# Optimization experiments

Hardware: AMD Instinct MI355X
Metric: run time of the kernel (lower is better)

## Reference

```python
import jax, jax.numpy as jnp
import numpy as np

N = 50000      # nodes
E = 800000     # edges
T = 3          # npass
ED = 64        # embedding_dim
NS = 23        # nshifts (arange(0.8, 3.0+1e-5, 0.1))
MD = NS + ED   # message_dim = 87
H = 200        # hidden width (hardcoded in module)
NMOL = 2048    # number of molecules (segments for final scatter)
RD = ED * (T + 1)  # readout input dim = 256
EPS = 1e-5

SHIFTS = jnp.asarray(np.arange(0.8, 3.0 + 1e-5, 0.1, dtype=np.float32))  # [23]


def setup_inputs() -> dict:
    key = jax.random.key(0)
    ks = jax.random.split(key, 32)
    inp = {
        'z_i': jax.random.randint(ks[0], (N,), 0, 10),
        'edge_index': jax.random.randint(ks[1], (2, E), 0, N),
        'dist_ij': jax.random.uniform(ks[2], (E, 1), dtype=jnp.float32) * 2.2 + 0.8,
        'mol_ind': jnp.sort(jax.random.randint(ks[3], (N,), 0, NMOL)),
        'emb': jax.random.normal(ks[4], (10, ED), dtype=jnp.float32),
        # per-pass update MLP params, stacked over T
        'up_bn_g': jnp.ones((T, MD), jnp.float32),
        'up_bn_b': jnp.zeros((T, MD), jnp.float32),
        'up_w1': jax.random.normal(ks[5], (T, MD, H), jnp.float32) * 0.05,
        'up_b1': jnp.zeros((T, H), jnp.float32),
        'up_w2': jax.random.normal(ks[6], (T, H, H), jnp.float32) * 0.05,
        'up_b2': jnp.zeros((T, H), jnp.float32),
        'up_w3': jax.random.normal(ks[7], (T, H, H), jnp.float32) * 0.05,
        'up_b3': jnp.zeros((T, H), jnp.float32),
        'up_w4': jax.random.normal(ks[8], (T, H, ED), jnp.float32) * 0.05,
        'up_b4': jnp.zeros((T, ED), jnp.float32),
        # readout MLP params
        'ro_bn_g': jnp.ones((RD,), jnp.float32),
        'ro_bn_b': jnp.zeros((RD,), jnp.float32),
        'ro_w1': jax.random.normal(ks[9], (RD, H), jnp.float32) * 0.05,
        'ro_b1': jnp.zeros((H,), jnp.float32),
        'ro_w2': jax.random.normal(ks[10], (H, H), jnp.float32) * 0.05,
        'ro_b2': jnp.zeros((H,), jnp.float32),
        'ro_w3': jax.random.normal(ks[11], (H, H), jnp.float32) * 0.05,
        'ro_b3': jnp.zeros((H,), jnp.float32),
        'ro_w4': jax.random.normal(ks[12], (H, 1), jnp.float32) * 0.05,
        'ro_b4': jnp.zeros((1,), jnp.float32),  # bias filled to 0 in __init__
    }
    return inp


def batchnorm(x, g, b):
    # BatchNorm1d in training mode: batch statistics, biased variance
    mu = jnp.mean(x, axis=0)
    var = jnp.mean(jnp.square(x - mu), axis=0)
    return (x - mu) * jax.lax.rsqrt(var + EPS) * g + b


def mlp(x, g, b, w1, b1, w2, b2, w3, b3, w4, b4):
    x = batchnorm(x, g, b)
    x = jax.nn.relu(x @ w1 + b1)
    x = jax.nn.relu(x @ w2 + b2)
    x = jax.nn.relu(x @ w3 + b3)
    return x @ w4 + b4


def reference(z_i, edge_index, dist_ij, mol_ind, emb,
              up_bn_g, up_bn_b, up_w1, up_b1, up_w2, up_b2, up_w3, up_b3, up_w4, up_b4,
              ro_bn_g, ro_bn_b, ro_w1, ro_b1, ro_w2, ro_b2, ro_w3, ro_b3, ro_w4, ro_b4):
    e_source, e_sink = edge_index[0], edge_index[1]
    rbf_ij = jnp.exp(-jnp.square(dist_ij - SHIFTS[None, :]))  # [E, NS]
    x_i = emb[z_i]                                            # [N, ED]
    x_list = [x_i]
    for t in range(T):
        m_ij = jnp.concatenate([rbf_ij, x_i[e_sink]], axis=1)  # [E, MD] gather
        m_i = jax.ops.segment_sum(m_ij, e_source, num_segments=N)  # scatter-sum
        x_i = x_i + 0.1 * mlp(m_i, up_bn_g[t], up_bn_b[t],
                              up_w1[t], up_b1[t], up_w2[t], up_b2[t],
                              up_w3[t], up_b3[t], up_w4[t], up_b4[t])
        x_list.append(x_i)
    x_all = jnp.concatenate(x_list, axis=1)  # [N, RD]
    y_i = mlp(x_all, ro_bn_g, ro_bn_b, ro_w1, ro_b1, ro_w2, ro_b2, ro_w3, ro_b3, ro_w4, ro_b4)
    y = jax.ops.segment_sum(y_i, mol_ind, num_segments=NMOL)  # [NMOL, 1]
    return y
```

## Files before the change

### kernel.cpp

```cpp
#include <hip/hip_runtime.h>
#include <hip/hip_bf16.h>
#include <type_traits>

#define NN 50000
#define NP 50048
#define EE 800000
#define TT 3
#define ED 64
#define NS 23
#define MD 87
#define HH 200
#define NMOL 2048
#define RD 256

#define SW 232
#define NPB2 512
#define SNB ((NN + 255) / 256)

typedef __attribute__((ext_vector_type(8))) short short8b;
typedef __attribute__((ext_vector_type(4))) float f32x4;

template <int V> using ic = std::integral_constant<int, V>;

__device__ __forceinline__ unsigned short f2bf(float f) {
  unsigned u = __float_as_uint(f);
  return (unsigned short)((u + 0x7fffu + ((u >> 16) & 1u)) >> 16);
}
__device__ __forceinline__ float ubf2f(unsigned short h) {
  return __uint_as_float(((unsigned)h) << 16);
}
__device__ __forceinline__ float bfp2f(unsigned p) {
  return __uint_as_float(p << 16) + __uint_as_float(p & 0xffff0000u);
}
__device__ __forceinline__ unsigned packsplit(float v) {
  unsigned short h = f2bf(v);
  unsigned short l = f2bf(v - ubf2f(h));
  return (unsigned)h | ((unsigned)l << 16);
}

struct WD { const float* src; short* dst; int K, N, Kpad, Npad, T; };
struct WDs { WD d[5]; };

__global__ __launch_bounds__(256) void wprep_kernel(WDs W) {
  WD w = W.d[blockIdx.y];
  int KB = w.Kpad >> 5, NT = w.Npad >> 4;
  int per = w.Npad * w.Kpad;
  int total = w.T * per;
  for (int idx = blockIdx.x * 256 + threadIdx.x; idx < total; idx += gridDim.x * 256) {
    int t = idx / per;
    int r = idx - t * per;
    int e = r & 7, lane = (r >> 3) & 63;
    int blk = r >> 9;
    int kb = blk % KB, tile = blk / KB;
    int ln = lane & 15, quad = lane >> 4;
    int n = tile * 16 + ln, k = kb * 32 + quad * 8 + e;
    float v = 0.f;
    if (k < w.K && n < w.N) v = w.src[((size_t)t * w.K + k) * w.N + n];
    unsigned short h = f2bf(v);
    unsigned short l = f2bf(v - ubf2f(h));
    size_t base = ((size_t)(t * NT + tile) * KB + kb) * 1024;
    w.dst[base + lane * 8 + e] = (short)h;
    w.dst[base + 512 + lane * 8 + e] = (short)l;
  }
}

__global__ __launch_bounds__(256) void wscale_kernel(const float* __restrict__ wsrc,
                                                     const float* __restrict__ na,
                                                     const float* __restrict__ nb,
                                                     const float* __restrict__ bsrc,
                                                     int K, int Kpad,
                                                     short* __restrict__ wsp,
                                                     float* __restrict__ bc) {
  int n = blockIdx.x;
  int k = threadIdx.x;
  int KB = Kpad >> 5;
  int tile = n >> 4, ln = n & 15;
  float contrib = 0.f;
  if (k < Kpad) {
    float v = 0.f;
    if (n < HH && k < K) {
      float w = wsrc[(size_t)k * HH + n];
      v = na[k] * w;
      contrib = nb[k] * w;
    }
    unsigned short h = f2bf(v);
    unsigned short l = f2bf(v - ubf2f(h));
    int kb = k >> 5, quad = (k & 31) >> 3, e = k & 7;
    int lane = quad * 16 + ln;
    size_t base = ((size_t)tile * KB + kb) * 1024;
    wsp[base + lane * 8 + e] = (short)h;
    wsp[base + 512 + lane * 8 + e] = (short)l;
  }
  __shared__ float sh[256];
  sh[k] = contrib;
  __syncthreads();
  for (int off = 128; off > 0; off >>= 1) {
    if (k < off) sh[k] += sh[k + off];
    __syncthreads();
  }
  if (k == 0) bc[n] = (n < HH ? bsrc[n] : 0.f) + sh[0];
}

__global__ __launch_bounds__(256) void emb_kernel(const int* __restrict__ z,
                                                  const float* __restrict__ emb,
                                                  unsigned* __restrict__ xp,
                                                  short* __restrict__ xq,
                                                  short* __restrict__ xqs) {
  int idx = blockIdx.x * 256 + threadIdx.x;
  if (idx >= NN * ED) return;
  int i = idx >> 6, d = idx & 63;
  unsigned pk = packsplit(emb[z[i] * ED + d]);
  xp[(size_t)i * RD + d] = pk;
  short h = (short)(pk & 0xffffu);
  xq[(size_t)i * RD + d] = h;
  xqs[(size_t)i * ED + d] = h;
}

__global__ __launch_bounds__(256) void hist_kernel(const int* __restrict__ src,
                                                   int* __restrict__ deg) {
  int e = blockIdx.x * 256 + threadIdx.x;
  if (e < EE) atomicAdd(&deg[src[e]], 1);
}

__global__ __launch_bounds__(256) void scanA_kernel(const int* __restrict__ deg,
                                                    int* __restrict__ Psum) {
  int i = blockIdx.x * 256 + threadIdx.x;
  int v = (i < NN) ? deg[i] : 0;
#pragma unroll
  for (int off = 32; off > 0; off >>= 1) v += __shfl_down(v, off, 64);
  __shared__ int ws[4];
  if ((threadIdx.x & 63) == 0) ws[threadIdx.x >> 6] = v;
  __syncthreads();
  if (threadIdx.x == 0) Psum[blockIdx.x] = ws[0] + ws[1] + ws[2] + ws[3];
}

__global__ __launch_bounds__(256) void scanB_kernel(const int* __restrict__ Psum,
                                                    int* __restrict__ Poff) {
  __shared__ int sh[256];
  int t = threadIdx.x;
  int v = (t < SNB) ? Psum[t] : 0;
  sh[t] = v;
  __syncthreads();
  for (int off = 1; off < 256; off <<= 1) {
    int u = (t >= off) ? sh[t - off] : 0;
    __syncthreads();
    sh[t] += u;
    __syncthreads();
  }
  if (t < SNB) Poff[t] = sh[t] - v;
}

__global__ __launch_bounds__(256) void scanC_kernel(const int* __restrict__ deg,
                                                    const int* __restrict__ Poff,
                                                    int* __restrict__ offs,
                                                    int* __restrict__ cursor) {
  __shared__ int sh[256];
  int t = threadIdx.x;
  int i = blockIdx.x * 256 + t;
  int v = (i < NN) ? deg[i] : 0;
  sh[t] = v;
  __syncthreads();
  for (int off = 1; off < 256; off <<= 1) {
    int u = (t >= off) ? sh[t - off] : 0;
    __syncthreads();
    sh[t] += u;
    __syncthreads();
  }
  int excl = Poff[blockIdx.x] + sh[t] - v;
  if (i < NN) {
    offs[i] = excl;
    cursor[i] = excl;
    if (i == NN - 1) offs[NN] = excl + v;
  }
}

__global__ __launch_bounds__(256) void scatter_kernel(const int* __restrict__ src,
                                                      const int* __restrict__ snk,
                                                      const float* __restrict__ dist,
                                                      int* __restrict__ cursor,
                                                      int* __restrict__ ssink,
                                                      float* __restrict__ sdist) {
  int e = blockIdx.x * 256 + threadIdx.x;
  if (e >= EE) return;
  int p = atomicAdd(&cursor[src[e]], 1);
  ssink[p] = snk[e];
  sdist[p] = dist[e];
}

template <bool RBF>
__global__ __launch_bounds__(256) void gather_kernel(const int* __restrict__ offs,
                                                     const int* __restrict__ ssink,
                                                     const float* __restrict__ sdist,
                                                     const short* __restrict__ xqs,
                                                     short* __restrict__ mh) {
  int node = blockIdx.x * 4 + (threadIdx.x >> 6);
  int lane = threadIdx.x & 63;
  if (node >= NN) return;
  float shift = (float)(0.8 + 0.1 * (double)lane);
  int e0 = offs[node], e1 = offs[node + 1];
  float ax0 = 0.f, ax1 = 0.f, ar0 = 0.f, ar1 = 0.f;
  int j = e0;
  for (; j + 4 <= e1; j += 4) {
    int s0 = ssink[j], s1 = ssink[j + 1], s2 = ssink[j + 2], s3 = ssink[j + 3];
    float x0 = ubf2f((unsigned short)xqs[(size_t)s0 * ED + lane]);
    float x1 = ubf2f((unsigned short)xqs[(size_t)s1 * ED + lane]);
    float x2 = ubf2f((unsigned short)xqs[(size_t)s2 * ED + lane]);
    float x3 = ubf2f((unsigned short)xqs[(size_t)s3 * ED + lane]);
    ax0 += x0 + x2;
    ax1 += x1 + x3;
    if (RBF && lane < NS) {
      float d0 = sdist[j], d1 = sdist[j + 1], d2 = sdist[j + 2], d3 = sdist[j + 3];
      float u0 = d0 - shift, u1 = d1 - shift, u2 = d2 - shift, u3 = d3 - shift;
      ar0 += __expf(-u0 * u0) + __expf(-u2 * u2);
      ar1 += __expf(-u1 * u1) + __expf(-u3 * u3);
    }
  }
  for (; j < e1; j++) {
    int s = ssink[j];
    ax0 += ubf2f((unsigned short)xqs[(size_t)s * ED + lane]);
    if (RBF && lane < NS) {
      float u = sdist[j] - shift;
      ar0 += __expf(-u * u);
    }
  }
  float accx = ax0 + ax1;
  if (RBF && lane < NS) mh[(size_t)node * 96 + lane] = (short)f2bf(ar0 + ar1);
  if (RBF && lane >= NS && lane < 32) mh[(size_t)node * 96 + 64 + lane] = 0;
  mh[(size_t)node * 96 + NS + lane] = (short)f2bf(accx);
}

template <int LD>
__global__ __launch_bounds__(256) void colstats_s16_kernel(const short* __restrict__ X,
                                                           float* __restrict__ P) {
  constexpr int CG = LD / 8;
  constexpr int RPB = 256 / CG;
  const int t = threadIdx.x;
  const int cg = t % CG, rin = t / CG;
  float s[8] = {0, 0, 0, 0, 0, 0, 0, 0}, q[8] = {0, 0, 0, 0, 0, 0, 0, 0};
  if (rin < RPB) {
    for (int r = blockIdx.x * RPB + rin; r < NN; r += gridDim.x * RPB) {
      union { uint4 v; short e[8]; } u;
      u.v = *(const uint4*)(X + (size_t)r * LD + cg * 8);
#pragma unroll
      for (int e = 0; e < 8; e++) {
        float f = ubf2f((unsigned short)u.e[e]);
        s[e] += f;
        q[e] += f * f;
      }
    }
  }
  __shared__ float sh[256][16];
#pragma unroll
  for (int e = 0; e < 8; e++) { sh[t][e] = s[e]; sh[t][8 + e] = q[e]; }
  __syncthreads();
  if (rin == 0) {
    for (int rr = 1; rr < RPB; rr++) {
      const float* o = sh[rr * CG + cg];
#pragma unroll
      for (int e = 0; e < 8; e++) { s[e] += o[e]; q[e] += o[8 + e]; }
    }
    float* Pb = P + blockIdx.x * 512;
#pragma unroll
    for (int e = 0; e < 8; e++) {
      Pb[cg * 8 + e] = s[e];
      Pb[256 + cg * 8 + e] = q[e];
    }
  }
}

__global__ __launch_bounds__(256) void bnfinal2_kernel(const float* __restrict__ P, int nblk,
                                                       const float* __restrict__ g,
                                                       const float* __restrict__ b, int ncols,
                                                       float* __restrict__ na,
                                                       float* __restrict__ nb) {
  int c = blockIdx.x;
  int t = threadIdx.x;
  float s = 0.f, q = 0.f;
  for (int i = t; i < nblk; i += 256) {
    s += P[i * 512 + c];
    q += P[i * 512 + 256 + c];
  }
#pragma unroll
  for (int off = 32; off > 0; off >>= 1) {
    s += __shfl_down(s, off, 64);
    q += __shfl_down(q, off, 64);
  }
  __shared__ float ws[4], wq[4];
  if ((t & 63) == 0) { ws[t >> 6] = s; wq[t >> 6] = q; }
  __syncthreads();
  if (t == 0) {
    s = ws[0] + ws[1] + ws[2] + ws[3];
    q = wq[0] + wq[1] + wq[2] + wq[3];
    if (c < ncols) {
      float mean = s / (float)NN;
      float var = q / (float)NN - mean * mean;
      float a = g[c] * rsqrtf(var + 1e-5f);
      na[c] = a;
      nb[c] = b[c] - mean * a;
    } else {
      na[c] = 0.f;
      nb[c] = 0.f;
    }
  }
}

template <bool READOUT>
__global__ __launch_bounds__(256, 4) void fused_kernel(
    const short* __restrict__ Agh,
    const short* __restrict__ W1p, const short* __restrict__ W2p,
    const short* __restrict__ W3p, const short* __restrict__ W4p,
    const float* __restrict__ b1, const float* __restrict__ b2,
    const float* __restrict__ b3, const float* __restrict__ b4,
    unsigned* __restrict__ xp, short* __restrict__ xq, short* __restrict__ xqs,
    int t, const float* __restrict__ w4ro, const int* __restrict__ mol,
    float* __restrict__ out) {
  __shared__ short lds[4 * 16 * SW];
  constexpr int GLDA = READOUT ? RD : 96;
  constexpr int KB1 = READOUT ? 8 : 3;
  const int tid = threadIdx.x;
  const int wave = tid >> 6, lane = tid & 63, ln = lane & 15, quad = lane >> 4;
  const int q8 = quad * 8;
  const int bm = (blockIdx.x * 4 + wave) * 16;
  short* ldsW = lds + wave * (16 * SW);
  const short* aRow = ldsW + ln * SW;

#pragma unroll
  for (int p = 0; p < 6; p++) {
    int idx = p * 64 + lane;
    ldsW[(idx / 24) * SW + 208 + (idx % 24)] = 0;
  }

  f32x4 acc[2];
  auto pair = [&](auto kbt, auto tt, const short8b* a, const short* __restrict__ Wp,
                  int j0, int nj) {
    constexpr int KB = decltype(kbt)::value;
    constexpr int TERMS = decltype(tt)::value;
#pragma unroll
    for (int jj = 0; jj < 2; jj++) acc[jj] = (f32x4){0.f, 0.f, 0.f, 0.f};
#pragma unroll
    for (int kb = 0; kb < KB; kb++)
#pragma unroll
      for (int jj = 0; jj < 2; jj++)
        if (jj < nj) {
          const short* bp = Wp + (size_t)((j0 + jj) * KB + kb) * 1024 + lane * 8;
          acc[jj] = __builtin_amdgcn_mfma_f32_16x16x32_bf16(a[kb], *(const short8b*)bp,
                                                            acc[jj], 0, 0, 0);
          if constexpr (TERMS == 2)
            acc[jj] = __builtin_amdgcn_mfma_f32_16x16x32_bf16(
                a[kb], *(const short8b*)(bp + 512), acc[jj], 0, 0, 0);
        }
  };
  auto epi = [&](int j, const f32x4& ac, const float* __restrict__ bias) {
    int colg = j * 16 + ln;
    float bb = (colg < HH) ? bias[colg] : 0.f;
#pragma unroll
    for (int r = 0; r < 4; r++)
      ldsW[(quad * 4 + r) * SW + colg] = (short)f2bf(fmaxf(ac[r] + bb, 0.f));
  };

  {
    short8b a1[KB1];
#pragma unroll
    for (int kb = 0; kb < KB1; kb++)
      a1[kb] = *(const short8b*)(Agh + (size_t)(bm + ln) * GLDA + kb * 32 + q8);
#pragma unroll
    for (int j0 = 0; j0 < 13; j0 += 2) {
      int nj = (13 - j0 >= 2) ? 2 : 1;
      pair(ic<KB1>{}, ic<2>{}, a1, W1p, j0, nj);
      epi(j0, acc[0], b1);
      if (nj == 2) epi(j0 + 1, acc[1], b1);
    }
  }
  short8b a[7];
#pragma unroll
  for (int kb = 0; kb < 7; kb++)
    a[kb] = *(const short8b*)(aRow + kb * 32 + q8);

#pragma unroll
  for (int j0 = 0; j0 < 13; j0 += 2) {
    int nj = (13 - j0 >= 2) ? 2 : 1;
    pair(ic<7>{}, ic<1>{}, a, W2p, j0, nj);
    epi(j0, acc[0], b2);
    if (nj == 2) epi(j0 + 1, acc[1], b2);
  }
#pragma unroll
  for (int kb = 0; kb < 7; kb++)
    a[kb] = *(const short8b*)(aRow + kb * 32 + q8);

#pragma unroll
  for (int j0 = 0; j0 < 13; j0 += 2) {
    int nj = (13 - j0 >= 2) ? 2 : 1;
    pair(ic<7>{}, ic<1>{}, a, W3p, j0, nj);
    epi(j0, acc[0], b3);
    if (nj == 2) epi(j0 + 1, acc[1], b3);
  }
#pragma unroll
  for (int kb = 0; kb < 7; kb++)
    a[kb] = *(const short8b*)(aRow + kb * 32 + q8);

  if constexpr (!READOUT) {
#pragma unroll
    for (int j0 = 0; j0 < 4; j0 += 2) {
      pair(ic<7>{}, ic<2>{}, a, W4p, j0, 2);
#pragma unroll
      for (int jj = 0; jj < 2; jj++) {
        int colg = (j0 + jj) * 16 + ln;
        float bb = b4[colg];
#pragma unroll
        for (int r = 0; r < 4; r++) {
          int grow = bm + quad * 4 + r;
          if (grow < NN) {
            size_t base = (size_t)grow * RD;
            float oldv = bfp2f(xp[base + (size_t)t * ED + colg]);
            unsigned pk = packsplit(oldv + 0.1f * (acc[jj][r] + bb));
            xp[base + (size_t)(t + 1) * ED + colg] = pk;
            short h = (short)(pk & 0xffffu);
            xq[base + (size_t)(t + 1) * ED + colg] = h;
            xqs[(size_t)(t + 1) * NN * ED + (size_t)grow * ED + colg] = h;
          }
        }
      }
    }
  } else {
    float s = 0.f;
#pragma unroll
    for (int kb = 0; kb < 7; kb++)
      if (kb * 32 + q8 < HH)
#pragma unroll
        for (int e = 0; e < 8; e++)
          s += ubf2f((unsigned short)a[kb][e]) * w4ro[kb * 32 + q8 + e];
    s += __shfl_xor(s, 16, 64);
    s += __shfl_xor(s, 32, 64);
    int grow = bm + ln;
    if (lane < 16 && grow < NN) atomicAdd(&out[mol[grow]], s + b4[0]);
  }
}

extern "C" void kernel_launch(void* const* d_in, const int* in_sizes, int n_in,
                              void* d_out, int out_size, void* d_ws, size_t ws_size,
                              hipStream_t stream) {
  const int* z_i = (const int*)d_in[0];
  const int* e_src = (const int*)d_in[1];
  const int* e_snk = ((const int*)d_in[1]) + EE;
  const float* dist = (const float*)d_in[2];
  const int* mol = (const int*)d_in[3];
  const float* emb = (const float*)d_in[4];
  const float* up_bn_g = (const float*)d_in[5];
  const float* up_bn_b = (const float*)d_in[6];
  const float* up_w1 = (const float*)d_in[7];
  const float* up_b1 = (const float*)d_in[8];
  const float* up_w2 = (const float*)d_in[9];
  const float* up_b2 = (const float*)d_in[10];
  const float* up_w3 = (const float*)d_in[11];
  const float* up_b3 = (const float*)d_in[12];
  const float* up_w4 = (const float*)d_in[13];
  const float* up_b4 = (const float*)d_in[14];
  const float* ro_bn_g = (const float*)d_in[15];
  const float* ro_bn_b = (const float*)d_in[16];
  const float* ro_w1 = (const float*)d_in[17];
  const float* ro_b1 = (const float*)d_in[18];
  const float* ro_w2 = (const float*)d_in[19];
  const float* ro_b2 = (const float*)d_in[20];
  const float* ro_w3 = (const float*)d_in[21];
  const float* ro_b3 = (const float*)d_in[22];
  const float* ro_w4 = (const float*)d_in[23];
  const float* ro_b4 = (const float*)d_in[24];
  float* out = (float*)d_out;

  char* p = (char*)d_ws;
  auto alloc = [&](size_t bytes) {
    void* r = (void*)p;
    p += (bytes + 255) & ~(size_t)255;
    return r;
  };
  unsigned* x_p = (unsigned*)alloc((size_t)NN * RD * 4);
  short* x_q = (short*)alloc((size_t)NP * RD * 2);
  short* x_qs = (short*)alloc((size_t)(TT + 1) * NN * ED * 2);
  short* mh = (short*)alloc((size_t)NP * 96 * 2);
  int* ssink = (int*)alloc((size_t)EE * 4);
  float* sdist = (float*)alloc((size_t)EE * 4);
  int* offs = (int*)alloc((size_t)(NN + 1) * 4);
  int* deg = (int*)alloc((size_t)NN * 4);
  int* cursor = (int*)alloc((size_t)NN * 4);
  int* Psum = (int*)alloc((size_t)SNB * 4);
  int* Poff = (int*)alloc((size_t)SNB * 4);
  float* P = (float*)alloc((size_t)NPB2 * 512 * 4);
  float* na = (float*)alloc(256 * 4);
  float* nb = (float*)alloc(256 * 4);
  float* b1c = (float*)alloc(208 * 4);
  short* w1sp = (short*)alloc((size_t)13 * 3 * 1024 * 2);
  short* r1sp = (short*)alloc((size_t)13 * 8 * 1024 * 2);
  short* w2p = (short*)alloc((size_t)TT * 13 * 7 * 1024 * 2);
  short* w3p = (short*)alloc((size_t)TT * 13 * 7 * 1024 * 2);
  short* w4p = (short*)alloc((size_t)TT * 4 * 7 * 1024 * 2);
  short* r2p = (short*)alloc((size_t)13 * 7 * 1024 * 2);
  short* r3p = (short*)alloc((size_t)13 * 7 * 1024 * 2);

  hipMemsetAsync(deg, 0, (size_t)NN * 4, stream);
  hipMemsetAsync(out, 0, (size_t)NMOL * 4, stream);

  WDs descs;
  descs.d[0] = {up_w2, w2p, HH, HH, 224, 208, TT};
  descs.d[1] = {up_w3, w3p, HH, HH, 224, 208, TT};
  descs.d[2] = {up_w4, w4p, HH, ED, 224, 64, TT};
  descs.d[3] = {ro_w2, r2p, HH, HH, 224, 208, 1};
  descs.d[4] = {ro_w3, r3p, HH, HH, 224, 208, 1};
  wprep_kernel<<<dim3(546, 5), 256, 0, stream>>>(descs);

  emb_kernel<<<(NN * ED + 255) / 256, 256, 0, stream>>>(z_i, emb, x_p, x_q, x_qs);
  hist_kernel<<<(EE + 255) / 256, 256, 0, stream>>>(e_src, deg);
  scanA_kernel<<<SNB, 256, 0, stream>>>(deg, Psum);
  scanB_kernel<<<1, 256, 0, stream>>>(Psum, Poff);
  scanC_kernel<<<SNB, 256, 0, stream>>>(deg, Poff, offs, cursor);
  scatter_kernel<<<(EE + 255) / 256, 256, 0, stream>>>(e_src, e_snk, dist, cursor, ssink, sdist);

  const int gM = NP / 64;

  for (int t = 0; t < TT; t++) {
    if (t == 0)
      gather_kernel<true><<<(NN + 3) / 4, 256, 0, stream>>>(
          offs, ssink, sdist, x_qs, mh);
    else
      gather_kernel<false><<<(NN + 3) / 4, 256, 0, stream>>>(
          offs, ssink, sdist, x_qs + (size_t)t * NN * ED, mh);
    colstats_s16_kernel<96><<<NPB2, 256, 0, stream>>>(mh, P);
    bnfinal2_kernel<<<256, 256, 0, stream>>>(P, NPB2, up_bn_g + t * MD, up_bn_b + t * MD, MD,
                                             na, nb);
    wscale_kernel<<<208, 256, 0, stream>>>(up_w1 + (size_t)t * MD * HH, na, nb,
                                           up_b1 + t * HH, MD, 96, w1sp, b1c);
    fused_kernel<false><<<gM, 256, 0, stream>>>(
        mh, w1sp,
        w2p + (size_t)t * 13 * 7 * 1024, w3p + (size_t)t * 13 * 7 * 1024,
        w4p + (size_t)t * 4 * 7 * 1024,
        b1c, up_b2 + t * HH, up_b3 + t * HH, up_b4 + t * ED,
        x_p, x_q, x_qs, t, nullptr, nullptr, nullptr);
  }

  colstats_s16_kernel<256><<<NPB2, 256, 0, stream>>>(x_q, P);
  bnfinal2_kernel<<<256, 256, 0, stream>>>(P, NPB2, ro_bn_g, ro_bn_b, RD, na, nb);
  wscale_kernel<<<208, 256, 0, stream>>>(ro_w1, na, nb, ro_b1, RD, 256, r1sp, b1c);
  fused_kernel<true><<<gM, 256, 0, stream>>>(
      x_q, r1sp, r2p, r3p, nullptr,
      b1c, ro_b2, ro_b3, ro_b4,
      nullptr, nullptr, nullptr, 0, ro_w4, mol, out);

  (void)in_sizes; (void)n_in; (void)out_size; (void)ws_size;
}
```

Measured before the change: 606.7 us.

## Use single-wave blocks and widen MFMA column groups in fused MLP kernel

Turns the fused MLP kernel into one-wave blocks of 16 rows (64 threads, grid NP/16) with a private LDS tile per block. Each layer now runs as two wide passes of 7 and 6 column tiles instead of pairs of 2, and all B fragments for a k-step are loaded before the MFMAs issue, so more loads are in flight and MFMA chains are longer. This adds register pressure (7 accumulators plus 7 B fragments), and launch bounds drop to 64 threads with 3 blocks. Occupancy and scheduling change substantially.

```diff
diff --git a/kernel.cpp b/kernel.cpp
--- a/kernel.cpp
+++ b/kernel.cpp
@@ -305,7 +305,7 @@
 }
 
 template <bool READOUT>
-__global__ __launch_bounds__(256, 4) void fused_kernel(
+__global__ __launch_bounds__(64, 3) void fused_kernel(
     const short* __restrict__ Agh,
     const short* __restrict__ W1p, const short* __restrict__ W2p,
     const short* __restrict__ W3p, const short* __restrict__ W4p,
@@ -314,14 +314,12 @@
     unsigned* __restrict__ xp, short* __restrict__ xq, short* __restrict__ xqs,
     int t, const float* __restrict__ w4ro, const int* __restrict__ mol,
     float* __restrict__ out) {
-  __shared__ short lds[4 * 16 * SW];
+  __shared__ short ldsW[16 * SW];
   constexpr int GLDA = READOUT ? RD : 96;
   constexpr int KB1 = READOUT ? 8 : 3;
-  const int tid = threadIdx.x;
-  const int wave = tid >> 6, lane = tid & 63, ln = lane & 15, quad = lane >> 4;
-  const int q8 = quad * 8;
-  const int bm = (blockIdx.x * 4 + wave) * 16;
-  short* ldsW = lds + wave * (16 * SW);
+  const int lane = threadIdx.x;
+  const int ln = lane & 15, quad = lane >> 4, q8 = quad * 8;
+  const int bm = blockIdx.x * 16;
   const short* aRow = ldsW + ln * SW;
 
 #pragma unroll
@@ -330,32 +328,54 @@
     ldsW[(idx / 24) * SW + 208 + (idx % 24)] = 0;
   }
 
-  f32x4 acc[2];
-  auto pair = [&](auto kbt, auto tt, const short8b* a, const short* __restrict__ Wp,
-                  int j0, int nj) {
+  f32x4 acc[7];
+  short8b a[7];
+
+  auto mat = [&](auto ntt, auto kbt, auto tt, const short8b* af,
+                 const short* __restrict__ Wp, int j0) {
+    constexpr int NT = decltype(ntt)::value;
     constexpr int KB = decltype(kbt)::value;
     constexpr int TERMS = decltype(tt)::value;
 #pragma unroll
-    for (int jj = 0; jj < 2; jj++) acc[jj] = (f32x4){0.f, 0.f, 0.f, 0.f};
-#pragma unroll
-    for (int kb = 0; kb < KB; kb++)
-#pragma unroll
-      for (int jj = 0; jj < 2; jj++)
-        if (jj < nj) {
-          const short* bp = Wp + (size_t)((j0 + jj) * KB + kb) * 1024 + lane * 8;
-          acc[jj] = __builtin_amdgcn_mfma_f32_16x16x32_bf16(a[kb], *(const short8b*)bp,
-                                                            acc[jj], 0, 0, 0);
-          if constexpr (TERMS == 2)
-            acc[jj] = __builtin_amdgcn_mfma_f32_16x16x32_bf16(
-                a[kb], *(const short8b*)(bp + 512), acc[jj], 0, 0, 0);
-        }
+    for (int j = 0; j < NT; j++) acc[j] = (f32x4){0.f, 0.f, 0.f, 0.f};
+#pragma unroll
+    for (int kb = 0; kb < KB; kb++) {
+      short8b bh[NT];
+#pragma unroll
+      for (int j = 0; j < NT; j++)
+        bh[j] = *(const short8b*)(Wp + (size_t)((j0 + j) * KB + kb) * 1024 + lane * 8);
+#pragma unroll
+      for (int j = 0; j < NT; j++)
+        acc[j] = __builtin_amdgcn_mfma_f32_16x16x32_bf16(af[kb], bh[j], acc[j], 0, 0, 0);
+    }
+    if constexpr (TERMS == 2) {
+#pragma unroll
+      for (int kb = 0; kb < KB; kb++) {
+        short8b bl[NT];
+#pragma unroll
+        for (int j = 0; j < NT; j++)
+          bl[j] = *(const short8b*)(Wp + (size_t)((j0 + j) * KB + kb) * 1024 + 512 + lane * 8);
+#pragma unroll
+        for (int j = 0; j < NT; j++)
+          acc[j] = __builtin_amdgcn_mfma_f32_16x16x32_bf16(af[kb], bl[j], acc[j], 0, 0, 0);
+      }
+    }
   };
-  auto epi = [&](int j, const f32x4& ac, const float* __restrict__ bias) {
-    int colg = j * 16 + ln;
-    float bb = (colg < HH) ? bias[colg] : 0.f;
-#pragma unroll
-    for (int r = 0; r < 4; r++)
-      ldsW[(quad * 4 + r) * SW + colg] = (short)f2bf(fmaxf(ac[r] + bb, 0.f));
+  auto epi = [&](auto ntt, int j0, const float* __restrict__ bias) {
+    constexpr int NT = decltype(ntt)::value;
+#pragma unroll
+    for (int j = 0; j < NT; j++) {
+      int colg = (j0 + j) * 16 + ln;
+      float bb = (colg < HH) ? bias[colg] : 0.f;
+#pragma unroll
+      for (int r = 0; r < 4; r++)
+        ldsW[(quad * 4 + r) * SW + colg] = (short)f2bf(fmaxf(acc[j][r] + bb, 0.f));
+    }
+  };
+  auto loadA = [&]() {
+#pragma unroll
+    for (int kb = 0; kb < 7; kb++)
+      a[kb] = *(const short8b*)(aRow + kb * 32 + q8);
   };
 
   {
@@ -363,61 +383,43 @@
 #pragma unroll
     for (int kb = 0; kb < KB1; kb++)
       a1[kb] = *(const short8b*)(Agh + (size_t)(bm + ln) * GLDA + kb * 32 + q8);
-#pragma unroll
-    for (int j0 = 0; j0 < 13; j0 += 2) {
-      int nj = (13 - j0 >= 2) ? 2 : 1;
-      pair(ic<KB1>{}, ic<2>{}, a1, W1p, j0, nj);
-      epi(j0, acc[0], b1);
-      if (nj == 2) epi(j0 + 1, acc[1], b1);
-    }
-  }
-  short8b a[7];
-#pragma unroll
-  for (int kb = 0; kb < 7; kb++)
-    a[kb] = *(const short8b*)(aRow + kb * 32 + q8);
-
-#pragma unroll
-  for (int j0 = 0; j0 < 13; j0 += 2) {
-    int nj = (13 - j0 >= 2) ? 2 : 1;
-    pair(ic<7>{}, ic<1>{}, a, W2p, j0, nj);
-    epi(j0, acc[0], b2);
-    if (nj == 2) epi(j0 + 1, acc[1], b2);
-  }
-#pragma unroll
-  for (int kb = 0; kb < 7; kb++)
-    a[kb] = *(const short8b*)(aRow + kb * 32 + q8);
-
-#pragma unroll
-  for (int j0 = 0; j0 < 13; j0 += 2) {
-    int nj = (13 - j0 >= 2) ? 2 : 1;
-    pair(ic<7>{}, ic<1>{}, a, W3p, j0, nj);
-    epi(j0, acc[0], b3);
-    if (nj == 2) epi(j0 + 1, acc[1], b3);
-  }
-#pragma unroll
-  for (int kb = 0; kb < 7; kb++)
-    a[kb] = *(const short8b*)(aRow + kb * 32 + q8);
+    mat(ic<7>{}, ic<KB1>{}, ic<2>{}, a1, W1p, 0);
+    epi(ic<7>{}, 0, b1);
+    mat(ic<6>{}, ic<KB1>{}, ic<2>{}, a1, W1p, 7);
+    epi(ic<6>{}, 7, b1);
+  }
+
+  loadA();
+  mat(ic<7>{}, ic<7>{}, ic<1>{}, a, W2p, 0);
+  epi(ic<7>{}, 0, b2);
+  mat(ic<6>{}, ic<7>{}, ic<1>{}, a, W2p, 7);
+  epi(ic<6>{}, 7, b2);
+
+  loadA();
+  mat(ic<7>{}, ic<7>{}, ic<1>{}, a, W3p, 0);
+  epi(ic<7>{}, 0, b3);
+  mat(ic<6>{}, ic<7>{}, ic<1>{}, a, W3p, 7);
+  epi(ic<6>{}, 7, b3);
+
+  loadA();
 
   if constexpr (!READOUT) {
-#pragma unroll
-    for (int j0 = 0; j0 < 4; j0 += 2) {
-      pair(ic<7>{}, ic<2>{}, a, W4p, j0, 2);
-#pragma unroll
-      for (int jj = 0; jj < 2; jj++) {
-        int colg = (j0 + jj) * 16 + ln;
-        float bb = b4[colg];
-#pragma unroll
-        for (int r = 0; r < 4; r++) {
-          int grow = bm + quad * 4 + r;
-          if (grow < NN) {
-            size_t base = (size_t)grow * RD;
-            float oldv = bfp2f(xp[base + (size_t)t * ED + colg]);
-            unsigned pk = packsplit(oldv + 0.1f * (acc[jj][r] + bb));
-            xp[base + (size_t)(t + 1) * ED + colg] = pk;
-            short h = (short)(pk & 0xffffu);
-            xq[base + (size_t)(t + 1) * ED + colg] = h;
-            xqs[(size_t)(t + 1) * NN * ED + (size_t)grow * ED + colg] = h;
-          }
+    mat(ic<4>{}, ic<7>{}, ic<2>{}, a, W4p, 0);
+#pragma unroll
+    for (int j = 0; j < 4; j++) {
+      int colg = j * 16 + ln;
+      float bb = b4[colg];
+#pragma unroll
+      for (int r = 0; r < 4; r++) {
+        int grow = bm + quad * 4 + r;
+        if (grow < NN) {
+          size_t base = (size_t)grow * RD;
+          float oldv = bfp2f(xp[base + (size_t)t * ED + colg]);
+          unsigned pk = packsplit(oldv + 0.1f * (acc[j][r] + bb));
+          xp[base + (size_t)(t + 1) * ED + colg] = pk;
+          short h = (short)(pk & 0xffffu);
+          xq[base + (size_t)(t + 1) * ED + colg] = h;
+          xqs[(size_t)(t + 1) * NN * ED + (size_t)grow * ED + colg] = h;
         }
       }
     }
@@ -514,7 +516,7 @@
   scanC_kernel<<<SNB, 256, 0, stream>>>(deg, Poff, offs, cursor);
   scatter_kernel<<<(EE + 255) / 256, 256, 0, stream>>>(e_src, e_snk, dist, cursor, ssink, sdist);
 
-  const int gM = NP / 64;
+  const int gM = NP / 16;
 
   for (int t = 0; t < TT; t++) {
     if (t == 0)
@@ -528,7 +530,7 @@
                                              na, nb);
     wscale_kernel<<<208, 256, 0, stream>>>(up_w1 + (size_t)t * MD * HH, na, nb,
                                            up_b1 + t * HH, MD, 96, w1sp, b1c);
-    fused_kernel<false><<<gM, 256, 0, stream>>>(
+    fused_kernel<false><<<gM, 64, 0, stream>>>(
         mh, w1sp,
         w2p + (size_t)t * 13 * 7 * 1024, w3p + (size_t)t * 13 * 7 * 1024,
         w4p + (size_t)t * 4 * 7 * 1024,
@@ -539,7 +541,7 @@
   colstats_s16_kernel<256><<<NPB2, 256, 0, stream>>>(x_q, P);
   bnfinal2_kernel<<<256, 256, 0, stream>>>(P, NPB2, ro_bn_g, ro_bn_b, RD, na, nb);
   wscale_kernel<<<208, 256, 0, stream>>>(ro_w1, na, nb, ro_b1, RD, 256, r1sp, b1c);
-  fused_kernel<true><<<gM, 256, 0, stream>>>(
+  fused_kernel<true><<<gM, 64, 0, stream>>>(
       x_q, r1sp, r2p, r3p, nullptr,
       b1c, ro_b2, ro_b3, ro_b4,
       nullptr, nullptr, nullptr, 0, ro_w4, mol, out);
```

Result: slower. 631.0 us (+4.0%).
